# Kernel optimization log

Hardware: AMD Instinct MI355X
Metric: run time of the kernel (lower is better)

Reference implementation:

```python
import jax, jax.numpy as jnp
import numpy as np

COV_EMB = 32
N_HEAD = 2
FACTOR_TCL = 2   # TemporalConvolutionalLayer factor (default 2)
FACTOR_MLP = 1   # MLP factor passed from MultiAttention init
EPS = 1e-5


def _conv1d_causal(x, w, b):
    # x: [N, C, T], w: [O, C, 3]; torch pads 2 both sides then slices [..., :-2],
    # equivalent to left-pad 2 only -> output length T.
    y = jax.lax.conv_general_dilated(x, w, window_strides=(1,), padding=[(2, 0)],
                                     dimension_numbers=('NCH', 'OIH', 'NCH'))
    return y + b[None, :, None]


def _tcl(x, w_conv, b_conv, w_proj, b_proj):
    # TemporalConvolutionalLayer: x [..., T, C] -> [..., T, C]
    shp = x.shape
    T, C = shp[-2], shp[-1]
    x2 = x.reshape(-1, T, C).transpose(0, 2, 1)              # [N, C, T]
    h = jax.nn.gelu(_conv1d_causal(x2, w_conv, b_conv), approximate=False)
    h = h.transpose(0, 2, 1)                                  # [N, T, 2C]
    out = h @ w_proj.T + b_proj                               # [N, T, C]
    return out.reshape(*shp[:-1], C)


def _layernorm(x, w):
    mu = jnp.mean(x, axis=-1, keepdims=True)
    var = jnp.var(x, axis=-1, keepdims=True)
    return (x - mu) * jax.lax.rsqrt(var + EPS) * w


def setup_inputs() -> dict:
    key = jax.random.key(0)
    ks = jax.random.split(key, 20)
    C = COV_EMB
    C2 = FACTOR_TCL * C
    s = 0.02
    inp = {
        'causal_decoder': jax.random.normal(ks[0], (8, 4, 1024, C), jnp.float32),
        'past_kv': jax.random.normal(ks[1], (8, 1024, C), jnp.float32),
    }
    def tcl_params(i):
        return (jax.random.normal(ks[i], (C2, C, 3), jnp.float32) * s,
                jnp.zeros((C2,), jnp.float32),
                jax.random.normal(ks[i + 1], (C, C2), jnp.float32) * s,
                jnp.zeros((C,), jnp.float32))
    inp['wq_conv'], inp['bq_conv'], inp['wq_proj'], inp['bq_proj'] = tcl_params(2)
    inp['wk_conv'], inp['bk_conv'], inp['wk_proj'], inp['bk_proj'] = tcl_params(4)
    inp['wv_conv'], inp['bv_conv'], inp['wv_proj'], inp['bv_proj'] = tcl_params(6)
    inp['w_cproj'] = jax.random.normal(ks[8], (C, C), jnp.float32) * s   # bias=False
    inp['ln_w'] = jnp.ones((C,), jnp.float32)                            # bias=False
    inp['w_fc'] = jax.random.normal(ks[9], (FACTOR_MLP * C, C), jnp.float32) * s   # bias=False
    inp['w_mlp_proj'] = jax.random.normal(ks[10], (C, FACTOR_MLP * C), jnp.float32) * s
    return inp


def reference(causal_decoder, past_kv,
              wq_conv, bq_conv, wq_proj, bq_proj,
              wk_conv, bk_conv, wk_proj, bk_proj,
              wv_conv, bv_conv, wv_proj, bv_proj,
              w_cproj, ln_w, w_fc, w_mlp_proj):
    B, F, T, C = causal_decoder.shape
    nh, hd = N_HEAD, C // N_HEAD

    q = _tcl(causal_decoder, wq_conv, bq_conv, wq_proj, bq_proj)   # [B,F,T,C]
    k = _tcl(past_kv, wk_conv, bk_conv, wk_proj, bk_proj)          # [B,S,C]
    v = _tcl(past_kv, wv_conv, bv_conv, wv_proj, bv_proj)          # [B,S,C]

    S = k.shape[1]
    q = q.reshape(B, F, T, nh, hd).transpose(0, 1, 3, 2, 4)        # [B,F,h,T,d]
    k = k.reshape(B, S, nh, hd).transpose(0, 2, 1, 3)              # [B,h,S,d]
    v = v.reshape(B, S, nh, hd).transpose(0, 2, 1, 3)              # [B,h,S,d]

    scale = 1.0 / jnp.sqrt(jnp.asarray(hd, q.dtype))
    scores = jnp.einsum('bfhtd,bhsd->bfhts', q, k) * scale          # [B,F,h,T,S]
    attn = jax.nn.softmax(scores, axis=-1)
    y = jnp.einsum('bfhts,bhsd->bfhtd', attn, v)                    # [B,F,h,T,d]
    y = y.transpose(0, 1, 3, 2, 4).reshape(B, F, T, C)

    out = causal_decoder + y @ w_cproj.T                            # resid_dropout = id (p=0)
    h = _layernorm(out, ln_w)
    mlp = jax.nn.gelu(h @ w_fc.T, approximate=False) @ w_mlp_proj.T
    out = out + mlp
    return out
```

## Files before the change

### kernel.cpp

```cpp
#include <hip/hip_runtime.h>
#include <hip/hip_bf16.h>

#define T_LEN 1024

typedef __attribute__((ext_vector_type(8))) short short8;
typedef __attribute__((ext_vector_type(4))) short short4v;
typedef __attribute__((ext_vector_type(4))) float float4v;

__device__ __forceinline__ float gelu_exact(float x) {
    return 0.5f * x * (1.0f + erff(x * 0.70710678118654752440f));
}
__device__ __forceinline__ unsigned short f2bf(float f) {
    unsigned u = __float_as_uint(f);
    u += 0x7fffu + ((u >> 16) & 1u);
    return (unsigned short)(u >> 16);
}
__device__ __forceinline__ unsigned pk2bf(float a, float b) {
    __hip_bfloat162 h = __float22bfloat162_rn(make_float2(a, b));
    unsigned u;
    __builtin_memcpy(&u, &h, 4);
    return u;
}

__global__ __launch_bounds__(256) void kv_tcl(
    const float* __restrict__ pkv,
    const float* __restrict__ wkc, const float* __restrict__ bkc,
    const float* __restrict__ wkp, const float* __restrict__ bkp,
    const float* __restrict__ wvc, const float* __restrict__ bvc,
    const float* __restrict__ wvp, const float* __restrict__ bvp,
    unsigned short* __restrict__ kbf, unsigned short* __restrict__ vtbf)
{
    __shared__ __align__(16) unsigned short Abuf[32 * 96];
    __shared__ __align__(16) unsigned short WbT[64 * 96];
    __shared__ __align__(16) unsigned short Hb[32 * 72];
    __shared__ __align__(16) unsigned short WpB[32 * 72];

    const int tid = threadIdx.x;
    const int gb = blockIdx.x;

    const float *wc, *bc, *wp, *bp;
    unsigned short* outb;
    int n, mode;
    if (gb < 256) { n = gb >> 5;         wc = wkc; bc = bkc; wp = wkp; bp = bkp; outb = kbf;  mode = 0; }
    else          { n = (gb - 256) >> 5; wc = wvc; bc = bvc; wp = wvp; bp = bvp; outb = vtbf; mode = 1; }
    const int t0 = (gb & 31) * 32;

#pragma unroll
    for (int it = 0; it < 3; ++it) {
        int s = (tid + it * 256) >> 3;
        int sub = tid & 7;
        int t = s / 3, tap = s - t * 3;
        int tau = t0 + t - 2 + tap;
        float4 xv = make_float4(0.f, 0.f, 0.f, 0.f);
        if (tau >= 0) xv = *(const float4*)&pkv[((size_t)n * T_LEN + tau) * 32 + sub * 4];
        short4v pk = { (short)f2bf(xv.x), (short)f2bf(xv.y),
                       (short)f2bf(xv.z), (short)f2bf(xv.w) };
        *(short4v*)&Abuf[t * 96 + tap * 32 + sub * 4] = pk;
    }
#pragma unroll
    for (int it = 0; it < 6; ++it) {
        int i4 = tid + it * 256;
        int idx = i4 * 4;
        int o = idx / 96, r = idx - o * 96;
        float4 w4 = *(const float4*)&wc[idx];
        float we[4] = { w4.x, w4.y, w4.z, w4.w };
#pragma unroll
        for (int e = 0; e < 4; ++e) {
            int re = r + e, c = re / 3, tap = re - c * 3;
            WbT[o * 96 + tap * 32 + c] = f2bf(we[e]);
        }
    }
#pragma unroll
    for (int it = 0; it < 2; ++it) {
        int i4 = tid + it * 256;
        int idx = i4 * 4;
        int c = idx >> 6, o = idx & 63;
        float4 w4 = *(const float4*)&wp[idx];
        short4v pk = { (short)f2bf(w4.x), (short)f2bf(w4.y),
                       (short)f2bf(w4.z), (short)f2bf(w4.w) };
        *(short4v*)&WpB[c * 72 + o] = pk;
    }

    const int w = tid >> 6;
    const int ln = tid & 63;
    const int sn = ln & 15;
    const int quad = ln >> 4;

    const float bcv = bc[w * 16 + sn];
    const int tmw = w & 1, cnw = w >> 1;
    const float bpv = bp[cnw * 16 + sn];

    __syncthreads();

    short8 b0 = *(const short8*)&WbT[(w * 16 + sn) * 96 + 0  + quad * 8];
    short8 b1 = *(const short8*)&WbT[(w * 16 + sn) * 96 + 32 + quad * 8];
    short8 b2 = *(const short8*)&WbT[(w * 16 + sn) * 96 + 64 + quad * 8];
    float4v zero = { 0.f, 0.f, 0.f, 0.f };
    float4v acc[2] = { zero, zero };
#pragma unroll
    for (int tm = 0; tm < 2; ++tm) {
        const unsigned short* ar = &Abuf[(tm * 16 + sn) * 96 + quad * 8];
        short8 a0 = *(const short8*)(ar + 0);
        short8 a1 = *(const short8*)(ar + 32);
        short8 a2 = *(const short8*)(ar + 64);
        acc[tm] = __builtin_amdgcn_mfma_f32_16x16x32_bf16(a0, b0, acc[tm], 0, 0, 0);
        acc[tm] = __builtin_amdgcn_mfma_f32_16x16x32_bf16(a1, b1, acc[tm], 0, 0, 0);
        acc[tm] = __builtin_amdgcn_mfma_f32_16x16x32_bf16(a2, b2, acc[tm], 0, 0, 0);
    }
#pragma unroll
    for (int tm = 0; tm < 2; ++tm) {
        float ge[4];
        ge[0] = gelu_exact(acc[tm].x + bcv);
        ge[1] = gelu_exact(acc[tm].y + bcv);
        ge[2] = gelu_exact(acc[tm].z + bcv);
        ge[3] = gelu_exact(acc[tm].w + bcv);
#pragma unroll
        for (int i = 0; i < 4; ++i)
            Hb[(tm * 16 + quad * 4 + i) * 72 + w * 16 + sn] = f2bf(ge[i]);
    }

    __syncthreads();

    const unsigned short* hr = &Hb[(tmw * 16 + sn) * 72 + quad * 8];
    short8 pa0 = *(const short8*)(hr + 0);
    short8 pa1 = *(const short8*)(hr + 32);
    short8 pb0 = *(const short8*)&WpB[(cnw * 16 + sn) * 72 + quad * 8];
    short8 pb1 = *(const short8*)&WpB[(cnw * 16 + sn) * 72 + 32 + quad * 8];
    float4v pacc = zero;
    pacc = __builtin_amdgcn_mfma_f32_16x16x32_bf16(pa0, pb0, pacc, 0, 0, 0);
    pacc = __builtin_amdgcn_mfma_f32_16x16x32_bf16(pa1, pb1, pacc, 0, 0, 0);

    float v[4] = { pacc.x + bpv, pacc.y + bpv, pacc.z + bpv, pacc.w + bpv };
#pragma unroll
    for (int i = 0; i < 4; ++i) {
        int t = tmw * 16 + quad * 4 + i;
        int c = cnw * 16 + sn;
        if (mode == 0) {
            outb[((size_t)n * T_LEN + t0 + t) * 32 + c] = f2bf(v[i]);
        } else {
            outb[((size_t)(n * 2 + cnw) * 16 + sn) * T_LEN + t0 + t] = f2bf(v[i]);
        }
    }
}

__global__ __launch_bounds__(512) void fused_qae(
    const float* __restrict__ cd,
    const float* __restrict__ wqc, const float* __restrict__ bqc,
    const float* __restrict__ wqp, const float* __restrict__ bqp,
    const unsigned short* __restrict__ kbf,
    const unsigned short* __restrict__ vtbf,
    const float* __restrict__ wcp, const float* __restrict__ lnw,
    const float* __restrict__ wfc, const float* __restrict__ wmp,
    float* __restrict__ out)
{
    __shared__ __align__(16) char smem[30208];
    unsigned short* Abuf = (unsigned short*)(smem);
    unsigned short* WbT  = (unsigned short*)(smem + 6144);
    unsigned short* Hb   = (unsigned short*)(smem + 18432);
    unsigned short* WpB  = (unsigned short*)(smem + 23040);
    unsigned short* qs   = (unsigned short*)(smem + 27648);
    unsigned short* plds = (unsigned short*)(smem);

    const int tid = threadIdx.x;
    const int bf = blockIdx.x >> 5;
    const int tt = blockIdx.x & 31;
    const int t0 = tt * 32;
    const int b = bf >> 2;
    const float SC = 0.36067376022224085f;

#pragma unroll
    for (int it = 0; it < 2; ++it) {
        int idx = tid + it * 512;
        if (idx < 768) {
            int s = idx >> 3;
            int sub = idx & 7;
            int t = s / 3, tap = s - t * 3;
            int tau = t0 + t - 2 + tap;
            float4 xv = make_float4(0.f, 0.f, 0.f, 0.f);
            if (tau >= 0) xv = *(const float4*)&cd[((size_t)bf * T_LEN + tau) * 32 + sub * 4];
            short4v pk = { (short)f2bf(xv.x), (short)f2bf(xv.y),
                           (short)f2bf(xv.z), (short)f2bf(xv.w) };
            *(short4v*)&Abuf[t * 96 + tap * 32 + sub * 4] = pk;
        }
    }
#pragma unroll
    for (int it = 0; it < 3; ++it) {
        int i4 = tid + it * 512;
        int idx = i4 * 4;
        int o = idx / 96, r = idx - o * 96;
        float4 w4 = *(const float4*)&wqc[idx];
        float we[4] = { w4.x, w4.y, w4.z, w4.w };
#pragma unroll
        for (int e = 0; e < 4; ++e) {
            int re = r + e, c = re / 3, tap = re - c * 3;
            WbT[o * 96 + tap * 32 + c] = f2bf(we[e]);
        }
    }
    {
        int idx = tid * 4;
        int c = idx >> 6, o = idx & 63;
        float4 w4 = *(const float4*)&wqp[idx];
        short4v pk = { (short)f2bf(w4.x), (short)f2bf(w4.y),
                       (short)f2bf(w4.z), (short)f2bf(w4.w) };
        *(short4v*)&WpB[c * 72 + o] = pk;
    }

    const int w = tid >> 6;
    const int ln = tid & 63;
    const int sn = ln & 15;
    const int quad = ln >> 4;
    const float4v zero = { 0.f, 0.f, 0.f, 0.f };

    __syncthreads();

    {
        const int tm = w & 1, on = w >> 1;
        const unsigned short* ar = &Abuf[(tm * 16 + sn) * 96 + quad * 8];
        short8 a0 = *(const short8*)(ar + 0);
        short8 a1 = *(const short8*)(ar + 32);
        short8 a2 = *(const short8*)(ar + 64);
        const unsigned short* br = &WbT[(on * 16 + sn) * 96 + quad * 8];
        float4v c0 = zero;
        c0 = __builtin_amdgcn_mfma_f32_16x16x32_bf16(a0, *(const short8*)(br + 0),  c0, 0, 0, 0);
        c0 = __builtin_amdgcn_mfma_f32_16x16x32_bf16(a1, *(const short8*)(br + 32), c0, 0, 0, 0);
        c0 = __builtin_amdgcn_mfma_f32_16x16x32_bf16(a2, *(const short8*)(br + 64), c0, 0, 0, 0);
        const float bc0 = bqc[on * 16 + sn];
        float g0[4] = { gelu_exact(c0.x + bc0), gelu_exact(c0.y + bc0),
                        gelu_exact(c0.z + bc0), gelu_exact(c0.w + bc0) };
#pragma unroll
        for (int i = 0; i < 4; ++i)
            Hb[(tm * 16 + quad * 4 + i) * 72 + on * 16 + sn] = f2bf(g0[i]);
    }
    __syncthreads();

    if (w < 4) {
        const int tm = w & 1, cn = w >> 1;
        const unsigned short* hr = &Hb[(tm * 16 + sn) * 72 + quad * 8];
        short8 pa0 = *(const short8*)(hr + 0);
        short8 pa1 = *(const short8*)(hr + 32);
        const unsigned short* wr_ = &WpB[(cn * 16 + sn) * 72 + quad * 8];
        short8 pb0 = *(const short8*)(wr_ + 0);
        short8 pb1 = *(const short8*)(wr_ + 32);
        float4v pacc = zero;
        pacc = __builtin_amdgcn_mfma_f32_16x16x32_bf16(pa0, pb0, pacc, 0, 0, 0);
        pacc = __builtin_amdgcn_mfma_f32_16x16x32_bf16(pa1, pb1, pacc, 0, 0, 0);
        const float bpv = bqp[cn * 16 + sn];
        float v[4] = { (pacc.x + bpv) * SC, (pacc.y + bpv) * SC,
                       (pacc.z + bpv) * SC, (pacc.w + bpv) * SC };
#pragma unroll
        for (int i = 0; i < 4; ++i)
            qs[(tm * 16 + quad * 4 + i) * 40 + cn * 16 + sn] = f2bf(v[i]);
    }
    __syncthreads();

    const int h = w & 1, rt = (w >> 1) & 1, sh = w >> 2;
    short8 aq = {0, 0, 0, 0, 0, 0, 0, 0};
    if (quad < 2)
        aq = *(const short8*)&qs[(rt * 16 + sn) * 40 + h * 16 + quad * 8];

    const unsigned short* kb = kbf + (size_t)b * T_LEN * 32 + h * 16 + quad * 8;
    const unsigned short* vb = vtbf + ((size_t)(b * 2 + h) * 16 + sn) * T_LEN + quad * 8;
    unsigned short* pwA = plds + w * 1152;
    unsigned short* pwB = pwA + 576;

    float4v yacc = zero;
    float l0 = 0.f, l1 = 0.f, l2 = 0.f, l3 = 0.f;
    const int sbeg = sh * 512;

#pragma unroll 1
    for (int s0 = sbeg; s0 < sbeg + 512; s0 += 64) {
        short8 ka0 = {0,0,0,0,0,0,0,0}, ka1 = ka0, kb0 = ka0, kb1 = ka0;
        if (quad < 2) {
            ka0 = *(const short8*)(kb + (size_t)(s0 + sn) * 32);
            ka1 = *(const short8*)(kb + (size_t)(s0 + 16 + sn) * 32);
            kb0 = *(const short8*)(kb + (size_t)(s0 + 32 + sn) * 32);
            kb1 = *(const short8*)(kb + (size_t)(s0 + 48 + sn) * 32);
        }
        short8 bvA = *(const short8*)(vb + s0);
        short8 bvB = *(const short8*)(vb + s0 + 32);

        float4v cA0 = __builtin_amdgcn_mfma_f32_16x16x32_bf16(aq, ka0, zero, 0, 0, 0);
        float4v cA1 = __builtin_amdgcn_mfma_f32_16x16x32_bf16(aq, ka1, zero, 0, 0, 0);
        float4v cB0 = __builtin_amdgcn_mfma_f32_16x16x32_bf16(aq, kb0, zero, 0, 0, 0);
        float4v cB1 = __builtin_amdgcn_mfma_f32_16x16x32_bf16(aq, kb1, zero, 0, 0, 0);

        float a0x = exp2f(cA0.x), a0y = exp2f(cA0.y), a0z = exp2f(cA0.z), a0w = exp2f(cA0.w);
        float a1x = exp2f(cA1.x), a1y = exp2f(cA1.y), a1z = exp2f(cA1.z), a1w = exp2f(cA1.w);
        float b0x = exp2f(cB0.x), b0y = exp2f(cB0.y), b0z = exp2f(cB0.z), b0w = exp2f(cB0.w);
        float b1x = exp2f(cB1.x), b1y = exp2f(cB1.y), b1z = exp2f(cB1.z), b1w = exp2f(cB1.w);

        l0 += (a0x + a1x) + (b0x + b1x);
        l1 += (a0y + a1y) + (b0y + b1y);
        l2 += (a0z + a1z) + (b0z + b1z);
        l3 += (a0w + a1w) + (b0w + b1w);

        const int tb = quad * 4;
        unsigned uA0 = pk2bf(a0x, a1x), uA1 = pk2bf(a0y, a1y);
        unsigned uA2 = pk2bf(a0z, a1z), uA3 = pk2bf(a0w, a1w);
        unsigned uB0 = pk2bf(b0x, b1x), uB1 = pk2bf(b0y, b1y);
        unsigned uB2 = pk2bf(b0z, b1z), uB3 = pk2bf(b0w, b1w);
        pwA[(tb + 0) * 36 + sn]      = (unsigned short)uA0;
        pwA[(tb + 0) * 36 + 16 + sn] = (unsigned short)(uA0 >> 16);
        pwA[(tb + 1) * 36 + sn]      = (unsigned short)uA1;
        pwA[(tb + 1) * 36 + 16 + sn] = (unsigned short)(uA1 >> 16);
        pwA[(tb + 2) * 36 + sn]      = (unsigned short)uA2;
        pwA[(tb + 2) * 36 + 16 + sn] = (unsigned short)(uA2 >> 16);
        pwA[(tb + 3) * 36 + sn]      = (unsigned short)uA3;
        pwA[(tb + 3) * 36 + 16 + sn] = (unsigned short)(uA3 >> 16);
        pwB[(tb + 0) * 36 + sn]      = (unsigned short)uB0;
        pwB[(tb + 0) * 36 + 16 + sn] = (unsigned short)(uB0 >> 16);
        pwB[(tb + 1) * 36 + sn]      = (unsigned short)uB1;
        pwB[(tb + 1) * 36 + 16 + sn] = (unsigned short)(uB1 >> 16);
        pwB[(tb + 2) * 36 + sn]      = (unsigned short)uB2;
        pwB[(tb + 2) * 36 + 16 + sn] = (unsigned short)(uB2 >> 16);
        pwB[(tb + 3) * 36 + sn]      = (unsigned short)uB3;
        pwB[(tb + 3) * 36 + 16 + sn] = (unsigned short)(uB3 >> 16);

        const unsigned short* prA = pwA + sn * 36 + quad * 8;
        const unsigned short* prB = pwB + sn * 36 + quad * 8;
        short4v aloA = *(const short4v*)prA;
        short4v ahiA = *(const short4v*)(prA + 4);
        short4v aloB = *(const short4v*)prB;
        short4v ahiB = *(const short4v*)(prB + 4);
        short8 apA = {aloA.x, aloA.y, aloA.z, aloA.w, ahiA.x, ahiA.y, ahiA.z, ahiA.w};
        short8 apB = {aloB.x, aloB.y, aloB.z, aloB.w, ahiB.x, ahiB.y, ahiB.z, ahiB.w};

        yacc = __builtin_amdgcn_mfma_f32_16x16x32_bf16(apA, bvA, yacc, 0, 0, 0);
        yacc = __builtin_amdgcn_mfma_f32_16x16x32_bf16(apB, bvB, yacc, 0, 0, 0);
    }

#pragma unroll
    for (int off = 1; off < 16; off <<= 1) {
        l0 += __shfl_xor(l0, off); l1 += __shfl_xor(l1, off);
        l2 += __shfl_xor(l2, off); l3 += __shfl_xor(l3, off);
    }

    float* pbuf = (float*)(smem + 18432);
    float* lbuf = (float*)(smem + 22528);
    float* sy   = (float*)(smem + 22784);
    const int wj = w & 3;
    if (sh == 1) {
        *(float4*)(pbuf + wj * 256 + ln * 4) =
            make_float4(yacc.x, yacc.y, yacc.z, yacc.w);
        if (sn == 0) {
            lbuf[wj * 16 + quad * 4 + 0] = l0;
            lbuf[wj * 16 + quad * 4 + 1] = l1;
            lbuf[wj * 16 + quad * 4 + 2] = l2;
            lbuf[wj * 16 + quad * 4 + 3] = l3;
        }
    }
    __syncthreads();
    if (sh == 0) {
        float4 o = *(float4*)(pbuf + wj * 256 + ln * 4);
        yacc.x += o.x; yacc.y += o.y; yacc.z += o.z; yacc.w += o.w;
        l0 += lbuf[wj * 16 + quad * 4 + 0];
        l1 += lbuf[wj * 16 + quad * 4 + 1];
        l2 += lbuf[wj * 16 + quad * 4 + 2];
        l3 += lbuf[wj * 16 + quad * 4 + 3];
        const float i0 = 1.f / l0, i1 = 1.f / l1, i2 = 1.f / l2, i3 = 1.f / l3;
        const int r0 = rt * 16 + quad * 4;
        sy[(r0 + 0) * 32 + h * 16 + sn] = yacc.x * i0;
        sy[(r0 + 1) * 32 + h * 16 + sn] = yacc.y * i1;
        sy[(r0 + 2) * 32 + h * 16 + sn] = yacc.z * i2;
        sy[(r0 + 3) * 32 + h * 16 + sn] = yacc.w * i3;
    }

    float* swc = (float*)(smem + 0);
    float* swf = (float*)(smem + 4608);
    float* swm = (float*)(smem + 9216);
    float* sln = (float*)(smem + 13824);
    float* shn = (float*)(smem + 13952);
    float* sgv = (float*)(smem + 16256);
    for (int i = tid; i < 1024; i += 512) {
        int r = i >> 5, cc = i & 31;
        swc[r * 36 + cc] = wcp[i];
        swf[r * 36 + cc] = wfc[i];
        swm[r * 36 + cc] = wmp[i];
    }
    if (tid < 32) sln[tid] = lnw[tid];
    __syncthreads();

    const int rl = tid >> 5, c = tid & 31;
    const float lnwc = sln[c];
#pragma unroll 1
    for (int p = 0; p < 2; ++p) {
        int r = p * 16 + rl;
        size_t row = (size_t)bf * T_LEN + t0 + r;
        float x1 = cd[row * 32 + c];
#pragma unroll
        for (int j4 = 0; j4 < 8; ++j4) {
            float4 yv = *(const float4*)&sy[r * 32 + j4 * 4];
            const float* wv = &swc[c * 36 + j4 * 4];
            x1 += wv[0] * yv.x + wv[1] * yv.y + wv[2] * yv.z + wv[3] * yv.w;
        }
        float s1 = x1, s2 = x1 * x1;
#pragma unroll
        for (int off = 16; off; off >>= 1) {
            s1 += __shfl_xor(s1, off);
            s2 += __shfl_xor(s2, off);
        }
        float mu = s1 * (1.0f / 32.0f);
        float var = s2 * (1.0f / 32.0f) - mu * mu;
        float hn = (x1 - mu) * rsqrtf(var + 1e-5f) * lnwc;
        shn[rl * 36 + c] = hn;
        float ga = 0.f;
#pragma unroll
        for (int j4 = 0; j4 < 8; ++j4) {
            float4 hv = *(const float4*)&shn[rl * 36 + j4 * 4];
            const float* wv = &swf[c * 36 + j4 * 4];
            ga += wv[0] * hv.x + wv[1] * hv.y + wv[2] * hv.z + wv[3] * hv.w;
        }
        float gv = gelu_exact(ga);
        sgv[rl * 36 + c] = gv;
        float oa = x1;
#pragma unroll
        for (int j4 = 0; j4 < 8; ++j4) {
            float4 gvv = *(const float4*)&sgv[rl * 36 + j4 * 4];
            const float* wv = &swm[c * 36 + j4 * 4];
            oa += wv[0] * gvv.x + wv[1] * gvv.y + wv[2] * gvv.z + wv[3] * gvv.w;
        }
        out[row * 32 + c] = oa;
    }
}

extern "C" void kernel_launch(void* const* d_in, const int* in_sizes, int n_in,
                              void* d_out, int out_size, void* d_ws, size_t ws_size,
                              hipStream_t stream) {
    const float* cd  = (const float*)d_in[0];
    const float* pkv = (const float*)d_in[1];
    const float* wqc = (const float*)d_in[2];
    const float* bqc = (const float*)d_in[3];
    const float* wqp = (const float*)d_in[4];
    const float* bqp = (const float*)d_in[5];
    const float* wkc = (const float*)d_in[6];
    const float* bkc = (const float*)d_in[7];
    const float* wkp = (const float*)d_in[8];
    const float* bkp = (const float*)d_in[9];
    const float* wvc = (const float*)d_in[10];
    const float* bvc = (const float*)d_in[11];
    const float* wvp = (const float*)d_in[12];
    const float* bvp = (const float*)d_in[13];
    const float* wcp = (const float*)d_in[14];
    const float* lnw = (const float*)d_in[15];
    const float* wfc = (const float*)d_in[16];
    const float* wmp = (const float*)d_in[17];

    unsigned short* kbf  = (unsigned short*)d_ws;
    unsigned short* vtbf = kbf + (size_t)8 * 1024 * 32;

    kv_tcl<<<512, 256, 0, stream>>>(pkv, wkc, bkc, wkp, bkp,
                                    wvc, bvc, wvp, bvp, kbf, vtbf);
    fused_qae<<<1024, 512, 0, stream>>>(cd, wqc, bqc, wqp, bqp, kbf, vtbf,
                                        wcp, lnw, wfc, wmp, (float*)d_out);
}
```

Measured before the change: 133.5 us.

## Interleave V-transpose key order to pack P stores as 32-bit LDS writes

The V-transpose producer now writes keys in an interleaved order within each 32-key block, so that positions s and s+16 sit next to each other. The attention loop can then store each pair of softmax probabilities as one packed 32-bit LDS write instead of two 16-bit writes, halving the store count. The K loads also drop the quad<2 guard, loading unconditionally and relying on the zeroed Q operand for the upper quads. The cost is extra index arithmetic in the producer and more global K loads per iteration.

```diff
diff --git a/kernel.cpp b/kernel.cpp
--- a/kernel.cpp
+++ b/kernel.cpp
@@ -138,7 +138,10 @@
         if (mode == 0) {
             outb[((size_t)n * T_LEN + t0 + t) * 32 + c] = f2bf(v[i]);
         } else {
-            outb[((size_t)(n * 2 + cnw) * 16 + sn) * T_LEN + t0 + t] = f2bf(v[i]);
+            int tloc = t0 + t;
+            int pos = tloc & 31;
+            int kp = ((pos & 15) << 1) | (pos >> 4);
+            outb[((size_t)(n * 2 + cnw) * 16 + sn) * T_LEN + (tloc & ~31) + kp] = f2bf(v[i]);
         }
     }
 }
@@ -269,20 +272,17 @@
 
 #pragma unroll 1
     for (int s0 = sbeg; s0 < sbeg + 512; s0 += 64) {
-        short8 ka0 = {0,0,0,0,0,0,0,0}, ka1 = ka0, kb0 = ka0, kb1 = ka0;
-        if (quad < 2) {
-            ka0 = *(const short8*)(kb + (size_t)(s0 + sn) * 32);
-            ka1 = *(const short8*)(kb + (size_t)(s0 + 16 + sn) * 32);
-            kb0 = *(const short8*)(kb + (size_t)(s0 + 32 + sn) * 32);
-            kb1 = *(const short8*)(kb + (size_t)(s0 + 48 + sn) * 32);
-        }
+        short8 ka0 = *(const short8*)(kb + (size_t)(s0 + sn) * 32);
+        short8 ka1 = *(const short8*)(kb + (size_t)(s0 + 16 + sn) * 32);
+        short8 kc0 = *(const short8*)(kb + (size_t)(s0 + 32 + sn) * 32);
+        short8 kc1 = *(const short8*)(kb + (size_t)(s0 + 48 + sn) * 32);
         short8 bvA = *(const short8*)(vb + s0);
         short8 bvB = *(const short8*)(vb + s0 + 32);
 
         float4v cA0 = __builtin_amdgcn_mfma_f32_16x16x32_bf16(aq, ka0, zero, 0, 0, 0);
         float4v cA1 = __builtin_amdgcn_mfma_f32_16x16x32_bf16(aq, ka1, zero, 0, 0, 0);
-        float4v cB0 = __builtin_amdgcn_mfma_f32_16x16x32_bf16(aq, kb0, zero, 0, 0, 0);
-        float4v cB1 = __builtin_amdgcn_mfma_f32_16x16x32_bf16(aq, kb1, zero, 0, 0, 0);
+        float4v cB0 = __builtin_amdgcn_mfma_f32_16x16x32_bf16(aq, kc0, zero, 0, 0, 0);
+        float4v cB1 = __builtin_amdgcn_mfma_f32_16x16x32_bf16(aq, kc1, zero, 0, 0, 0);
 
         float a0x = exp2f(cA0.x), a0y = exp2f(cA0.y), a0z = exp2f(cA0.z), a0w = exp2f(cA0.w);
         float a1x = exp2f(cA1.x), a1y = exp2f(cA1.y), a1z = exp2f(cA1.z), a1w = exp2f(cA1.w);
@@ -295,26 +295,14 @@
         l3 += (a0w + a1w) + (b0w + b1w);
 
         const int tb = quad * 4;
-        unsigned uA0 = pk2bf(a0x, a1x), uA1 = pk2bf(a0y, a1y);
-        unsigned uA2 = pk2bf(a0z, a1z), uA3 = pk2bf(a0w, a1w);
-        unsigned uB0 = pk2bf(b0x, b1x), uB1 = pk2bf(b0y, b1y);
-        unsigned uB2 = pk2bf(b0z, b1z), uB3 = pk2bf(b0w, b1w);
-        pwA[(tb + 0) * 36 + sn]      = (unsigned short)uA0;
-        pwA[(tb + 0) * 36 + 16 + sn] = (unsigned short)(uA0 >> 16);
-        pwA[(tb + 1) * 36 + sn]      = (unsigned short)uA1;
-        pwA[(tb + 1) * 36 + 16 + sn] = (unsigned short)(uA1 >> 16);
-        pwA[(tb + 2) * 36 + sn]      = (unsigned short)uA2;
-        pwA[(tb + 2) * 36 + 16 + sn] = (unsigned short)(uA2 >> 16);
-        pwA[(tb + 3) * 36 + sn]      = (unsigned short)uA3;
-        pwA[(tb + 3) * 36 + 16 + sn] = (unsigned short)(uA3 >> 16);
-        pwB[(tb + 0) * 36 + sn]      = (unsigned short)uB0;
-        pwB[(tb + 0) * 36 + 16 + sn] = (unsigned short)(uB0 >> 16);
-        pwB[(tb + 1) * 36 + sn]      = (unsigned short)uB1;
-        pwB[(tb + 1) * 36 + 16 + sn] = (unsigned short)(uB1 >> 16);
-        pwB[(tb + 2) * 36 + sn]      = (unsigned short)uB2;
-        pwB[(tb + 2) * 36 + 16 + sn] = (unsigned short)(uB2 >> 16);
-        pwB[(tb + 3) * 36 + sn]      = (unsigned short)uB3;
-        pwB[(tb + 3) * 36 + 16 + sn] = (unsigned short)(uB3 >> 16);
+        *(unsigned*)(pwA + (tb + 0) * 36 + sn * 2) = pk2bf(a0x, a1x);
+        *(unsigned*)(pwA + (tb + 1) * 36 + sn * 2) = pk2bf(a0y, a1y);
+        *(unsigned*)(pwA + (tb + 2) * 36 + sn * 2) = pk2bf(a0z, a1z);
+        *(unsigned*)(pwA + (tb + 3) * 36 + sn * 2) = pk2bf(a0w, a1w);
+        *(unsigned*)(pwB + (tb + 0) * 36 + sn * 2) = pk2bf(b0x, b1x);
+        *(unsigned*)(pwB + (tb + 1) * 36 + sn * 2) = pk2bf(b0y, b1y);
+        *(unsigned*)(pwB + (tb + 2) * 36 + sn * 2) = pk2bf(b0z, b1z);
+        *(unsigned*)(pwB + (tb + 3) * 36 + sn * 2) = pk2bf(b0w, b1w);
 
         const unsigned short* prA = pwA + sn * 36 + quad * 8;
         const unsigned short* prB = pwB + sn * 36 + quad * 8;
```

Result: slower. 138.4 us (+3.7%).
